# Performance work log

Hardware: AMD Instinct MI355X
Metric: run time of the kernel (lower is better)

Reference implementation:

```python
import jax, jax.numpy as jnp
import numpy as np

OBS, PRED, NAG, FIN, FOUT, H, NH, FF, NL = 8, 4, 256, 2, 2, 128, 8, 2048, 6


def _lin(x, w, b):
    return x @ w.T + b


def _ln(x, g, b, e=1e-5):
    m = x.mean(-1, keepdims=True)
    v = x.var(-1, keepdims=True)
    return (x - m) / jnp.sqrt(v + e) * g + b


def setup_inputs():
    key = jax.random.key(0)
    ks = iter(jax.random.split(key, 64))

    def w(shape, fan_in):
        return jax.random.normal(next(ks), shape, jnp.float32) / np.float32(np.sqrt(fan_in))

    return dict(
        traj_in=jax.random.normal(next(ks), (OBS + PRED, NAG, FIN), jnp.float32),
        adj_in=jax.random.uniform(next(ks), (OBS, NAG, NAG), jnp.float32),
        eps=jax.random.normal(next(ks), (OBS * NAG, H), jnp.float32),
        pro1_w=w((H, FIN), FIN), pro1_b=jnp.zeros(H, jnp.float32),
        pro2_w=w((H, H), H), pro2_b=jnp.zeros(H, jnp.float32),
        mu_w=w((H, H), H), mu_b=jnp.zeros(H, jnp.float32),
        ls_w=w((H, H), H), ls_b=jnp.zeros(H, jnp.float32),
        gdl_w=w((H, H), H), gdl_b=jnp.zeros(H, jnp.float32),
        pro3_w=w((H, OBS), OBS), pro3_b=jnp.zeros(H, jnp.float32),
        pro4_w=w((OBS, H), H), pro4_b=jnp.zeros(OBS, jnp.float32),
        pro5_w=w((FOUT, H), H), pro5_b=jnp.zeros(FOUT, jnp.float32),
        t_qkv_w=w((NL, 3 * H, H), H), t_qkv_b=jnp.zeros((NL, 3 * H), jnp.float32),
        t_out_w=w((NL, H, H), H), t_out_b=jnp.zeros((NL, H), jnp.float32),
        t_ff1_w=w((NL, FF, H), H), t_ff1_b=jnp.zeros((NL, FF), jnp.float32),
        t_ff2_w=w((NL, H, FF), FF), t_ff2_b=jnp.zeros((NL, H), jnp.float32),
        t_ln1_g=jnp.ones((NL, H), jnp.float32), t_ln1_b=jnp.zeros((NL, H), jnp.float32),
        t_ln2_g=jnp.ones((NL, H), jnp.float32), t_ln2_b=jnp.zeros((NL, H), jnp.float32),
        iftrain=1,
    )


def reference(traj_in, adj_in, eps, pro1_w, pro1_b, pro2_w, pro2_b, mu_w, mu_b,
              ls_w, ls_b, gdl_w, gdl_b, pro3_w, pro3_b, pro4_w, pro4_b,
              pro5_w, pro5_b, t_qkv_w, t_qkv_b, t_out_w, t_out_b,
              t_ff1_w, t_ff1_b, t_ff2_w, t_ff2_b, t_ln1_g, t_ln1_b,
              t_ln2_g, t_ln2_b, iftrain):
    batch_in = traj_in[:OBS, :, :FIN]            # [T, N, Fin]
    tar_y = traj_in[OBS:, :, :FOUT]              # [PRED, N, Fout]

    # block-diagonal adjacency over time, min-max normalized
    A = jax.scipy.linalg.block_diag(*[adj_in[t] for t in range(OBS)])  # [TN, TN]
    ADJ = (A - A.min()) / (A.max() - A.min())

    # GCNConv normalization: add remaining self-loops (weight 1), symmetric D^-1/2 A D^-1/2
    d = jnp.diagonal(ADJ)
    A_sl = ADJ + jnp.diag(jnp.where(d == 0, 1.0, 0.0).astype(ADJ.dtype))
    deg = A_sl.sum(0)
    dis = jnp.where(deg > 0, 1.0 / jnp.sqrt(deg), 0.0)
    agg = (dis[:, None] * A_sl * dis[None, :]).T  # aggregate src(row)->tgt(col)

    enc = _lin(jax.nn.relu(_lin(batch_in, pro1_w, pro1_b)), pro2_w, pro2_b)
    enc = enc.reshape(-1, H)                     # [TN, H]

    # VGAE encode (two GCNConv heads) + reparametrize, PyG clamps logstd at 10
    mu = agg @ _lin(enc, mu_w, mu_b)
    logstd = jnp.minimum(agg @ _lin(enc, ls_w, ls_b), 10.0)
    Z = jnp.where(jnp.asarray(iftrain) > 0, mu + eps * jnp.exp(logstd), mu)
    kld = -0.5 * jnp.mean(jnp.sum(1.0 + 2.0 * logstd - mu ** 2 - jnp.exp(2.0 * logstd), axis=1))

    out = _lin(Z, gdl_w, gdl_b)
    logits = Z @ Z.T                             # [TN, TN]
    struct_loss = jnp.mean(jnp.maximum(logits, 0.0) - logits * ADJ
                           + jnp.log1p(jnp.exp(-jnp.abs(logits))))

    # transformer over agents: [N, H, T] -> pro3 -> [N(seq), H(batch), H(d)]
    x = _lin(out.reshape(OBS, NAG, H).transpose(1, 2, 0), pro3_w, pro3_b)
    dh = H // NH
    S, B = x.shape[0], x.shape[1]
    for l in range(NL):
        qkv = _lin(x, t_qkv_w[l], t_qkv_b[l])
        q, k, v = jnp.split(qkv, 3, axis=-1)
        q = q.reshape(S, B, NH, dh)
        k = k.reshape(S, B, NH, dh)
        v = v.reshape(S, B, NH, dh)
        sc = jnp.einsum('sbhd,tbhd->bhst', q, k) / np.float32(np.sqrt(dh))
        att = jax.nn.softmax(sc, axis=-1)
        o = jnp.einsum('bhst,tbhd->sbhd', att, v).reshape(S, B, H)
        x = _ln(x + _lin(o, t_out_w[l], t_out_b[l]), t_ln1_g[l], t_ln1_b[l])
        f = _lin(jax.nn.relu(_lin(x, t_ff1_w[l], t_ff1_b[l])), t_ff2_w[l], t_ff2_b[l])
        x = _ln(x + f, t_ln2_g[l], t_ln2_b[l])

    out = _lin(x, pro4_w, pro4_b).transpose(2, 0, 1)   # [T, N, H]
    tra = _lin(out, pro5_w, pro5_b)                    # [T, N, Fout]
    traj = tra[-PRED:]
    traj_loss = jnp.sqrt(jnp.sum((traj - tar_y) ** 2, axis=-1)).sum(axis=0).mean()
    loss = traj_loss + kld + struct_loss
    return traj, loss
```

## Files before the change

### kernel.cpp

```cpp
#include <hip/hip_runtime.h>
#include <math.h>


namespace {

constexpr int kOBS = 8, kNAG = 256, kH = 128;
constexpr int kGN = kOBS * kNAG;
constexpr int kROWS = kNAG * kH;

typedef __attribute__((ext_vector_type(8))) short bf16x8;
typedef __attribute__((ext_vector_type(4))) float f32x4;
typedef __attribute__((ext_vector_type(4))) unsigned short us4;

struct Scal {
  int    mn_bits;
  int    mx_bits;
  float  Amin;
  float  invr;
  float  c0;
  int    pad;
  double kld_sum;
  double struct_sum;
  double traj_sum;
};

__device__ inline float waveReduceSum(float v) {
#pragma unroll
  for (int off = 32; off; off >>= 1) v += __shfl_xor(v, off, 64);
  return v;
}

__device__ inline unsigned short f2bf(float f) {
  unsigned u = __float_as_uint(f);
  return (unsigned short)((u + 0x7fffu + ((u >> 16) & 1u)) >> 16);
}
__device__ inline float bf2f(unsigned short h) {
  return __uint_as_float((unsigned)h << 16);
}
__device__ inline void split4(float4 v, us4& h, us4& l) {
  h.x = f2bf(v.x); l.x = f2bf(v.x - bf2f(h.x));
  h.y = f2bf(v.y); l.y = f2bf(v.y - bf2f(h.y));
  h.z = f2bf(v.z); l.z = f2bf(v.z - bf2f(h.z));
  h.w = f2bf(v.w); l.w = f2bf(v.w - bf2f(h.w));
}

__device__ inline int swz4(int c)  { return c ^ ((c >> 3) & 7); }
__device__ inline int swz16(int c) { return c ^ ((c >> 4) & 7); }

#define GLL(g, s)                                             \
  __builtin_amdgcn_global_load_lds(                           \
      (const __attribute__((address_space(1))) void*)(g),     \
      (__attribute__((address_space(3))) void*)(s), 16, 0, 0)

__global__ void k_init(Scal* sc) {
  if (threadIdx.x == 0) {
    sc->mn_bits = 0x7f800000;
    sc->mx_bits = 0xff800000;
    sc->kld_sum = 0.0;
    sc->struct_sum = 0.0;
    sc->traj_sum = 0.0;
  }
}

__global__ void k_minmax(const float* __restrict__ adj, int n, Scal* sc) {
  float lmin = INFINITY, lmax = -INFINITY;
  for (int i = blockIdx.x * blockDim.x + threadIdx.x; i < n;
       i += gridDim.x * blockDim.x) {
    float v = adj[i];
    lmin = fminf(lmin, v);
    lmax = fmaxf(lmax, v);
  }
#pragma unroll
  for (int off = 32; off; off >>= 1) {
    lmin = fminf(lmin, __shfl_xor(lmin, off, 64));
    lmax = fmaxf(lmax, __shfl_xor(lmax, off, 64));
  }
  __shared__ float smn[4], smx[4];
  int w = threadIdx.x >> 6;
  if ((threadIdx.x & 63) == 0) { smn[w] = lmin; smx[w] = lmax; }
  __syncthreads();
  if (threadIdx.x == 0) {
    lmin = fminf(fminf(smn[0], smn[1]), fminf(smn[2], smn[3]));
    lmax = fmaxf(fmaxf(smx[0], smx[1]), fmaxf(smx[2], smx[3]));
    atomicMin(&sc->mn_bits, __float_as_int(lmin));
    atomicMax(&sc->mx_bits, __float_as_int(lmax));
  }
}

__global__ void k_scale(Scal* sc) {
  float mn = fminf(0.0f, __int_as_float(sc->mn_bits));
  float mx = fmaxf(0.0f, __int_as_float(sc->mx_bits));
  sc->Amin = mn;
  sc->invr = 1.0f / (mx - mn);
  sc->c0 = (0.0f - mn) * sc->invr;
}

__global__ void k_dis(const float* __restrict__ adj, const Scal* __restrict__ sc,
                      float* __restrict__ dis) {
  int j = blockIdx.x * 256 + threadIdx.x;
  int t = j >> 8, jj = j & 255;
  const float* a = adj + (size_t)t * 65536;
  float Amin = sc->Amin, invr = sc->invr, c0 = sc->c0;
  float sum = 0.f;
  for (int i = 0; i < 256; ++i) sum += (a[i * 256 + jj] - Amin) * invr;
  float djj = (a[jj * 256 + jj] - Amin) * invr;
  float deg = sum + 1792.0f * c0 + (djj == 0.0f ? 1.0f : 0.0f);
  dis[j] = deg > 0.0f ? 1.0f / sqrtf(deg) : 0.0f;
}

__global__ void k_agg(const float* __restrict__ adj, const Scal* __restrict__ sc,
                      const float* __restrict__ dis, float* __restrict__ agg) {
  int idx = blockIdx.x * 256 + threadIdx.x;
  int t = idx >> 16, i = (idx >> 8) & 255, j = idx & 255;
  float v = (adj[(size_t)t * 65536 + j * 256 + i] - sc->Amin) * sc->invr;
  if (i == j && v == 0.0f) v += 1.0f;
  agg[idx] = dis[t * 256 + j] * v * dis[t * 256 + i];
}

__global__ void k_enc1(const float* __restrict__ traj, const float* __restrict__ w,
                       const float* __restrict__ b, float* __restrict__ out) {
  int idx = blockIdx.x * 256 + threadIdx.x;
  int r = idx >> 7, f = idx & 127;
  float v = traj[r * 2] * w[f * 2] + traj[r * 2 + 1] * w[f * 2 + 1] + b[f];
  out[idx] = fmaxf(v, 0.0f);
}

__global__ void k_cvt(const float* __restrict__ src, unsigned short* __restrict__ h,
                      unsigned short* __restrict__ l, int n4) {
  int i = blockIdx.x * 256 + threadIdx.x;
  if (i >= n4) return;
  float4 v = reinterpret_cast<const float4*>(src)[i];
  us4 hh, ll;
  split4(v, hh, ll);
  reinterpret_cast<us4*>(h)[i] = hh;
  reinterpret_cast<us4*>(l)[i] = ll;
}

#define BM 64
#define BN 64
#define KC 32
#define LP 68

template <bool TB>
__global__ __launch_bounds__(256) void gemm_kernel(
    const float* __restrict__ A, const float* __restrict__ B,
    const float* __restrict__ bias, float* __restrict__ C, int K, int ldb,
    int ldc, int flags, size_t aStride, size_t bStride, size_t cStride) {
  if (blockIdx.z) {
    A += (size_t)blockIdx.z * aStride;
    B += (size_t)blockIdx.z * bStride;
    C += (size_t)blockIdx.z * cStride;
  }
  __shared__ float As[KC][LP];
  __shared__ float Bs[KC][LP];
  const int tid = threadIdx.x;
  const int tx = tid & 15, ty = tid >> 4;
  const int m0 = blockIdx.y * BM, n0 = blockIdx.x * BN;
  float acc[4][4] = {};
  for (int k0 = 0; k0 < K; k0 += KC) {
#pragma unroll
    for (int i = 0; i < 2; ++i) {
      int q = tid + i * 256;
      int row = q >> 3, kq = q & 7;
      float4 v = *reinterpret_cast<const float4*>(
          &A[(size_t)(m0 + row) * K + k0 + kq * 4]);
      As[kq * 4 + 0][row] = v.x;
      As[kq * 4 + 1][row] = v.y;
      As[kq * 4 + 2][row] = v.z;
      As[kq * 4 + 3][row] = v.w;
    }
    if (TB) {
#pragma unroll
      for (int i = 0; i < 2; ++i) {
        int q = tid + i * 256;
        int row = q >> 3, kq = q & 7;
        float4 v = *reinterpret_cast<const float4*>(
            &B[(size_t)(n0 + row) * ldb + k0 + kq * 4]);
        Bs[kq * 4 + 0][row] = v.x;
        Bs[kq * 4 + 1][row] = v.y;
        Bs[kq * 4 + 2][row] = v.z;
        Bs[kq * 4 + 3][row] = v.w;
      }
    } else {
#pragma unroll
      for (int i = 0; i < 2; ++i) {
        int q = tid + i * 256;
        int kr = q >> 4, nq = q & 15;
        float4 v = *reinterpret_cast<const float4*>(
            &B[(size_t)(k0 + kr) * ldb + n0 + nq * 4]);
        *reinterpret_cast<float4*>(&Bs[kr][nq * 4]) = v;
      }
    }
    __syncthreads();
#pragma unroll
    for (int kk = 0; kk < KC; ++kk) {
      float4 a4 = *reinterpret_cast<const float4*>(&As[kk][ty * 4]);
      float4 b4 = *reinterpret_cast<const float4*>(&Bs[kk][tx * 4]);
      float av[4] = {a4.x, a4.y, a4.z, a4.w};
      float bv[4] = {b4.x, b4.y, b4.z, b4.w};
#pragma unroll
      for (int i = 0; i < 4; ++i)
#pragma unroll
        for (int j = 0; j < 4; ++j) acc[i][j] += av[i] * bv[j];
    }
    __syncthreads();
  }
  float bv[4] = {0.f, 0.f, 0.f, 0.f};
  if (bias) {
    float4 b4 = *reinterpret_cast<const float4*>(&bias[n0 + tx * 4]);
    bv[0] = b4.x; bv[1] = b4.y; bv[2] = b4.z; bv[3] = b4.w;
  }
#pragma unroll
  for (int i = 0; i < 4; ++i) {
    float* cp = &C[(size_t)(m0 + ty * 4 + i) * ldc + n0 + tx * 4];
    float4 o;
    float ov[4];
#pragma unroll
    for (int j = 0; j < 4; ++j) ov[j] = acc[i][j] + bv[j];
    if (flags & 2) {
      float4 old = *reinterpret_cast<const float4*>(cp);
      ov[0] += old.x; ov[1] += old.y; ov[2] += old.z; ov[3] += old.w;
    }
    if (flags & 1) {
#pragma unroll
      for (int j = 0; j < 4; ++j) ov[j] = fmaxf(ov[j], 0.0f);
    }
    o.x = ov[0]; o.y = ov[1]; o.z = ov[2]; o.w = ov[3];
    *reinterpret_cast<float4*>(cp) = o;
  }
}

template <int BMb, int BNb>
__global__ __launch_bounds__(256) void gemm_bf(
    const unsigned short* __restrict__ Ah, const unsigned short* __restrict__ Al,
    const unsigned short* __restrict__ Bh, const unsigned short* __restrict__ Bl,
    const float* __restrict__ bias, float* __restrict__ C,
    int K, int lda, int ldb, int ldc, int flags) {
  constexpr int MI = BMb / 32, NI = BNb / 32;
  constexpr int WTM = BMb / 2, WTN = BNb / 2;
  __shared__ unsigned short sAh[BMb * 32], sAl[BMb * 32];
  __shared__ unsigned short sBh[BNb * 32], sBl[BNb * 32];
  const int tid = threadIdx.x, lane = tid & 63, w = tid >> 6;
  const int wr = w >> 1, wc = w & 1;
  const int m0 = blockIdx.y * BMb, n0 = blockIdx.x * BNb;
  f32x4 acc[MI][NI];
#pragma unroll
  for (int i = 0; i < MI; ++i)
#pragma unroll
    for (int j = 0; j < NI; ++j) acc[i][j] = (f32x4){0.f, 0.f, 0.f, 0.f};

  for (int k0 = 0; k0 < K; k0 += 32) {
#pragma unroll
    for (int i = 0; i < BMb / 64; ++i) {
      int c = tid + i * 256;
      int g = swz4(c);
      int row = g >> 2, c4 = g & 3;
      size_t ga = (size_t)(m0 + row) * lda + k0 + c4 * 8;
      GLL(&Ah[ga], &sAh[c * 8]);
      GLL(&Al[ga], &sAl[c * 8]);
    }
#pragma unroll
    for (int i = 0; i < BNb / 64; ++i) {
      int c = tid + i * 256;
      int g = swz4(c);
      int row = g >> 2, c4 = g & 3;
      size_t ga = (size_t)(n0 + row) * ldb + k0 + c4 * 8;
      GLL(&Bh[ga], &sBh[c * 8]);
      GLL(&Bl[ga], &sBl[c * 8]);
    }
    __syncthreads();
    bf16x8 bh[NI], bl[NI];
#pragma unroll
    for (int ni = 0; ni < NI; ++ni) {
      int p = swz4((wc * WTN + ni * 16 + (lane & 15)) * 4 + (lane >> 4));
      bh[ni] = *reinterpret_cast<const bf16x8*>(&sBh[p * 8]);
      bl[ni] = *reinterpret_cast<const bf16x8*>(&sBl[p * 8]);
    }
#pragma unroll
    for (int mi = 0; mi < MI; ++mi) {
      int p = swz4((wr * WTM + mi * 16 + (lane & 15)) * 4 + (lane >> 4));
      bf16x8 ah = *reinterpret_cast<const bf16x8*>(&sAh[p * 8]);
      bf16x8 al = *reinterpret_cast<const bf16x8*>(&sAl[p * 8]);
#pragma unroll
      for (int ni = 0; ni < NI; ++ni) {
        acc[mi][ni] = __builtin_amdgcn_mfma_f32_16x16x32_bf16(
            ah, bh[ni], acc[mi][ni], 0, 0, 0);
        acc[mi][ni] = __builtin_amdgcn_mfma_f32_16x16x32_bf16(
            ah, bl[ni], acc[mi][ni], 0, 0, 0);
        acc[mi][ni] = __builtin_amdgcn_mfma_f32_16x16x32_bf16(
            al, bh[ni], acc[mi][ni], 0, 0, 0);
      }
    }
    __syncthreads();
  }
  const int crow0 = m0 + wr * WTM + (lane >> 4) * 4;
  const int ccol0 = n0 + wc * WTN + (lane & 15);
#pragma unroll
  for (int ni = 0; ni < NI; ++ni) {
    int col = ccol0 + ni * 16;
    float bv = bias ? bias[col] : 0.f;
#pragma unroll
    for (int mi = 0; mi < MI; ++mi) {
#pragma unroll
      for (int r = 0; r < 4; ++r) {
        int row = crow0 + mi * 16 + r;
        float v = acc[mi][ni][r] + bv;
        if (flags & 2) v += C[(size_t)row * ldc + col];
        if (flags & 1) v = fmaxf(v, 0.0f);
        C[(size_t)row * ldc + col] = v;
      }
    }
  }
}

__global__ __launch_bounds__(256) void k_ffn(
    const unsigned short* __restrict__ Xh, const unsigned short* __restrict__ Xl,
    const unsigned short* __restrict__ W1h, const unsigned short* __restrict__ W1l,
    const float* __restrict__ b1,
    const unsigned short* __restrict__ W2h, const unsigned short* __restrict__ W2l,
    const float* __restrict__ b2, float* __restrict__ out) {
  __shared__ unsigned short sXh[64 * 128], sXl[64 * 128];
  __shared__ unsigned short sW1h[32 * 128], sW1l[32 * 128];
  __shared__ unsigned short sPh[64 * 32], sPl[64 * 32];
  __shared__ unsigned short sW2h[128 * 32], sW2l[128 * 32];
  const int tid = threadIdx.x, lane = tid & 63, w = tid >> 6;
  const int wr = w >> 1, wc = w & 1;
  const int m0 = blockIdx.x * 64;
#pragma unroll
  for (int i = 0; i < 4; ++i) {
    int c = tid + i * 256;
    int g = swz16(c);
    size_t ga = (size_t)(m0 + (g >> 4)) * 128 + (g & 15) * 8;
    GLL(&Xh[ga], &sXh[c * 8]);
    GLL(&Xl[ga], &sXl[c * 8]);
  }
  __syncthreads();
  bf16x8 xah[4][2], xal[4][2];
#pragma unroll
  for (int ks = 0; ks < 4; ++ks)
#pragma unroll
    for (int mi = 0; mi < 2; ++mi) {
      int row = wr * 32 + mi * 16 + (lane & 15);
      int p = swz16(row * 16 + ks * 4 + (lane >> 4));
      xah[ks][mi] = *reinterpret_cast<const bf16x8*>(&sXh[p * 8]);
      xal[ks][mi] = *reinterpret_cast<const bf16x8*>(&sXl[p * 8]);
    }
  f32x4 acc2[2][4];
#pragma unroll
  for (int i = 0; i < 2; ++i)
#pragma unroll
    for (int j = 0; j < 4; ++j) acc2[i][j] = (f32x4){0.f, 0.f, 0.f, 0.f};

  const int pcol = wc * 16 + (lane & 15);
  for (int fc = 0; fc < 64; ++fc) {
    const int f0 = fc * 32;
#pragma unroll
    for (int i = 0; i < 2; ++i) {
      int c = tid + i * 256;
      {
        int g = swz16(c);
        size_t ga = (size_t)(f0 + (g >> 4)) * 128 + (g & 15) * 8;
        GLL(&W1h[ga], &sW1h[c * 8]);
        GLL(&W1l[ga], &sW1l[c * 8]);
      }
      {
        int g = swz4(c);
        size_t ga = (size_t)(g >> 2) * 2048 + f0 + (g & 3) * 8;
        GLL(&W2h[ga], &sW2h[c * 8]);
        GLL(&W2l[ga], &sW2l[c * 8]);
      }
    }
    __syncthreads();
    f32x4 acc1[2];
    acc1[0] = (f32x4){0.f, 0.f, 0.f, 0.f};
    acc1[1] = (f32x4){0.f, 0.f, 0.f, 0.f};
#pragma unroll
    for (int ks = 0; ks < 4; ++ks) {
      int p = swz16((wc * 16 + (lane & 15)) * 16 + ks * 4 + (lane >> 4));
      bf16x8 bh = *reinterpret_cast<const bf16x8*>(&sW1h[p * 8]);
      bf16x8 bl = *reinterpret_cast<const bf16x8*>(&sW1l[p * 8]);
#pragma unroll
      for (int mi = 0; mi < 2; ++mi) {
        acc1[mi] = __builtin_amdgcn_mfma_f32_16x16x32_bf16(xah[ks][mi], bh,
                                                           acc1[mi], 0, 0, 0);
        acc1[mi] = __builtin_amdgcn_mfma_f32_16x16x32_bf16(xah[ks][mi], bl,
                                                           acc1[mi], 0, 0, 0);
        acc1[mi] = __builtin_amdgcn_mfma_f32_16x16x32_bf16(xal[ks][mi], bh,
                                                           acc1[mi], 0, 0, 0);
      }
    }
    float b1v = b1[f0 + pcol];
#pragma unroll
    for (int mi = 0; mi < 2; ++mi)
#pragma unroll
      for (int r = 0; r < 4; ++r) {
        int prow = wr * 32 + mi * 16 + (lane >> 4) * 4 + r;
        float v = fmaxf(acc1[mi][r] + b1v, 0.0f);
        unsigned short h = f2bf(v);
        int p = swz4(prow * 4 + (pcol >> 3));
        sPh[p * 8 + (pcol & 7)] = h;
        sPl[p * 8 + (pcol & 7)] = f2bf(v - bf2f(h));
      }
    __syncthreads();
    bf16x8 pah[2], pal[2];
#pragma unroll
    for (int mi = 0; mi < 2; ++mi) {
      int p = swz4((wr * 32 + mi * 16 + (lane & 15)) * 4 + (lane >> 4));
      pah[mi] = *reinterpret_cast<const bf16x8*>(&sPh[p * 8]);
      pal[mi] = *reinterpret_cast<const bf16x8*>(&sPl[p * 8]);
    }
#pragma unroll
    for (int ni = 0; ni < 4; ++ni) {
      int p = swz4((wc * 64 + ni * 16 + (lane & 15)) * 4 + (lane >> 4));
      bf16x8 bh = *reinterpret_cast<const bf16x8*>(&sW2h[p * 8]);
      bf16x8 bl = *reinterpret_cast<const bf16x8*>(&sW2l[p * 8]);
#pragma unroll
      for (int mi = 0; mi < 2; ++mi) {
        acc2[mi][ni] = __builtin_amdgcn_mfma_f32_16x16x32_bf16(
            pah[mi], bh, acc2[mi][ni], 0, 0, 0);
        acc2[mi][ni] = __builtin_amdgcn_mfma_f32_16x16x32_bf16(
            pah[mi], bl, acc2[mi][ni], 0, 0, 0);
        acc2[mi][ni] = __builtin_amdgcn_mfma_f32_16x16x32_bf16(
            pal[mi], bh, acc2[mi][ni], 0, 0, 0);
      }
    }
    __syncthreads();
  }
#pragma unroll
  for (int ni = 0; ni < 4; ++ni) {
    int col = wc * 64 + ni * 16 + (lane & 15);
    float bv = b2[col];
#pragma unroll
    for (int mi = 0; mi < 2; ++mi)
#pragma unroll
      for (int r = 0; r < 4; ++r) {
        int row = m0 + wr * 32 + mi * 16 + (lane >> 4) * 4 + r;
        out[(size_t)row * 128 + col] = acc2[mi][ni][r] + bv;
      }
  }
}

__global__ void k_zkld(const float* __restrict__ mu, const float* __restrict__ lsr,
                       const float* __restrict__ eps, const int* __restrict__ iftrain,
                       float* __restrict__ Z, Scal* sc) {
  int i = blockIdx.x * 256 + threadIdx.x;
  float m = mu[i];
  float ls = fminf(lsr[i], 10.0f);
  float z = (*iftrain > 0) ? m + eps[i] * __expf(ls) : m;
  Z[i] = z;
  float kt = 1.0f + 2.0f * ls - m * m - __expf(2.0f * ls);
  kt = waveReduceSum(kt);
  __shared__ float sh[4];
  int w = threadIdx.x >> 6;
  if ((threadIdx.x & 63) == 0) sh[w] = kt;
  __syncthreads();
  if (threadIdx.x == 0)
    atomicAdd(&sc->kld_sum, (double)(sh[0] + sh[1] + sh[2] + sh[3]));
}

__global__ __launch_bounds__(256) void k_struct(const float* __restrict__ Z,
                                                const float* __restrict__ adj,
                                                Scal* sc) {
  __shared__ float As[KC][LP];
  __shared__ float Bs[KC][LP];
  const int tid = threadIdx.x;
  const int tx = tid & 15, ty = tid >> 4;
  const int m0 = blockIdx.y * BM, n0 = blockIdx.x * BN;
  float acc[4][4] = {};
  for (int k0 = 0; k0 < kH; k0 += KC) {
#pragma unroll
    for (int i = 0; i < 2; ++i) {
      int q = tid + i * 256;
      int row = q >> 3, kq = q & 7;
      float4 va = *reinterpret_cast<const float4*>(
          &Z[(size_t)(m0 + row) * kH + k0 + kq * 4]);
      As[kq * 4 + 0][row] = va.x;
      As[kq * 4 + 1][row] = va.y;
      As[kq * 4 + 2][row] = va.z;
      As[kq * 4 + 3][row] = va.w;
      float4 vb = *reinterpret_cast<const float4*>(
          &Z[(size_t)(n0 + row) * kH + k0 + kq * 4]);
      Bs[kq * 4 + 0][row] = vb.x;
      Bs[kq * 4 + 1][row] = vb.y;
      Bs[kq * 4 + 2][row] = vb.z;
      Bs[kq * 4 + 3][row] = vb.w;
    }
    __syncthreads();
#pragma unroll
    for (int kk = 0; kk < KC; ++kk) {
      float4 a4 = *reinterpret_cast<const float4*>(&As[kk][ty * 4]);
      float4 b4 = *reinterpret_cast<const float4*>(&Bs[kk][tx * 4]);
      float av[4] = {a4.x, a4.y, a4.z, a4.w};
      float bv[4] = {b4.x, b4.y, b4.z, b4.w};
#pragma unroll
      for (int i = 0; i < 4; ++i)
#pragma unroll
        for (int j = 0; j < 4; ++j) acc[i][j] += av[i] * bv[j];
    }
    __syncthreads();
  }
  float Amin = sc->Amin, invr = sc->invr, c0v = sc->c0;
  float lsum = 0.f;
#pragma unroll
  for (int i = 0; i < 4; ++i) {
#pragma unroll
    for (int j = 0; j < 4; ++j) {
      int gi = m0 + ty * 4 + i, gj = n0 + tx * 4 + j;
      float l = acc[i][j];
      float adjv = c0v;
      if ((gi >> 8) == (gj >> 8))
        adjv = (adj[((size_t)(gi >> 8) << 16) + (gi & 255) * 256 + (gj & 255)] -
                Amin) * invr;
      lsum += fmaxf(l, 0.0f) - l * adjv + __logf(1.0f + __expf(-fabsf(l)));
    }
  }
  lsum = waveReduceSum(lsum);
  __shared__ float sh[4];
  int w = threadIdx.x >> 6;
  if ((threadIdx.x & 63) == 0) sh[w] = lsum;
  __syncthreads();
  if (threadIdx.x == 0)
    atomicAdd(&sc->struct_sum, (double)(sh[0] + sh[1] + sh[2] + sh[3]));
}

__global__ void k_x0(const float* __restrict__ gdl, const float* __restrict__ w3,
                     const float* __restrict__ b3, float* __restrict__ X,
                     unsigned short* __restrict__ Xh,
                     unsigned short* __restrict__ Xl) {
  int f = threadIdx.x;
  size_t r = (size_t)blockIdx.x * 2 + threadIdx.y;
  int n = (int)(r >> 7), h = (int)(r & 127);
  float a = b3[f];
#pragma unroll
  for (int o = 0; o < 8; ++o)
    a += gdl[((size_t)o * 256 + n) * 128 + h] * w3[f * 8 + o];
  X[r * 128 + f] = a;
  unsigned short hh = f2bf(a);
  Xh[r * 128 + f] = hh;
  Xl[r * 128 + f] = f2bf(a - bf2f(hh));
}

__global__ __launch_bounds__(256) void k_attn(const float* __restrict__ QKV,
                                              unsigned short* __restrict__ Oh,
                                              unsigned short* __restrict__ Ol) {
  const int head = blockIdx.x, b = blockIdx.y;
  const int s = threadIdx.x;
  __shared__ float ks[256][16];
  __shared__ float vs[256][16];
  const size_t base = ((size_t)s * 128 + b) * 384 + head * 16;
#pragma unroll
  for (int i = 0; i < 4; ++i) {
    *reinterpret_cast<float4*>(&ks[s][i * 4]) =
        *reinterpret_cast<const float4*>(&QKV[base + 128 + i * 4]);
    *reinterpret_cast<float4*>(&vs[s][i * 4]) =
        *reinterpret_cast<const float4*>(&QKV[base + 256 + i * 4]);
  }
  float q[16];
#pragma unroll
  for (int i = 0; i < 4; ++i) {
    float4 v = *reinterpret_cast<const float4*>(&QKV[base + i * 4]);
    q[i * 4 + 0] = v.x * 0.25f; q[i * 4 + 1] = v.y * 0.25f;
    q[i * 4 + 2] = v.z * 0.25f; q[i * 4 + 3] = v.w * 0.25f;
  }
  __syncthreads();
  float m = -1e30f, lsum = 0.f;
  float o[16] = {};
#pragma unroll 2
  for (int t = 0; t < 256; ++t) {
    float kv[16], vv[16];
#pragma unroll
    for (int i = 0; i < 4; ++i) {
      float4 k4 = *reinterpret_cast<const float4*>(&ks[t][i * 4]);
      float4 v4 = *reinterpret_cast<const float4*>(&vs[t][i * 4]);
      kv[i * 4 + 0] = k4.x; kv[i * 4 + 1] = k4.y;
      kv[i * 4 + 2] = k4.z; kv[i * 4 + 3] = k4.w;
      vv[i * 4 + 0] = v4.x; vv[i * 4 + 1] = v4.y;
      vv[i * 4 + 2] = v4.z; vv[i * 4 + 3] = v4.w;
    }
    float d = 0.f;
#pragma unroll
    for (int i = 0; i < 16; ++i) d += q[i] * kv[i];
    if (d > m + 8.f) {
      float c = __expf(m - d);
      lsum *= c;
#pragma unroll
      for (int i = 0; i < 16; ++i) o[i] *= c;
      m = d;
    }
    float p = __expf(d - m);
    lsum += p;
#pragma unroll
    for (int i = 0; i < 16; ++i) o[i] += p * vv[i];
  }
  float inv = 1.0f / lsum;
  size_t ob = ((size_t)s * 128 + b) * 128 + head * 16;
#pragma unroll
  for (int i = 0; i < 4; ++i) {
    float4 v;
    v.x = o[i * 4 + 0] * inv; v.y = o[i * 4 + 1] * inv;
    v.z = o[i * 4 + 2] * inv; v.w = o[i * 4 + 3] * inv;
    us4 hh, ll;
    split4(v, hh, ll);
    *reinterpret_cast<us4*>(&Oh[ob + i * 4]) = hh;
    *reinterpret_cast<us4*>(&Ol[ob + i * 4]) = ll;
  }
}

__global__ __launch_bounds__(256) void k_resid_ln(
    float* __restrict__ X, const float* __restrict__ T,
    const float* __restrict__ g, const float* __restrict__ b,
    unsigned short* __restrict__ Xh, unsigned short* __restrict__ Xl) {
  int lane = threadIdx.x & 63, rl = threadIdx.x >> 6;
  size_t row = (size_t)blockIdx.x * 4 + rl;
  float* xp = X + row * 128;
  const float* tp = T + row * 128;
  float e0 = xp[lane] + tp[lane];
  float e1 = xp[lane + 64] + tp[lane + 64];
  float mean = waveReduceSum(e0 + e1) * 0.0078125f;
  float d0 = e0 - mean, d1 = e1 - mean;
  float var = waveReduceSum(d0 * d0 + d1 * d1) * 0.0078125f;
  float inv = 1.0f / sqrtf(var + 1e-5f);
  float v0 = d0 * inv * g[lane] + b[lane];
  float v1 = d1 * inv * g[lane + 64] + b[lane + 64];
  xp[lane] = v0;
  xp[lane + 64] = v1;
  unsigned short h0 = f2bf(v0), h1 = f2bf(v1);
  Xh[row * 128 + lane] = h0;
  Xl[row * 128 + lane] = f2bf(v0 - bf2f(h0));
  Xh[row * 128 + lane + 64] = h1;
  Xl[row * 128 + lane + 64] = f2bf(v1 - bf2f(h1));
}

__global__ void k_heady(const float* __restrict__ X, const float* __restrict__ w4,
                        const float* __restrict__ b4, float* __restrict__ y) {
  int tid = threadIdx.x;
  int o = tid & 7, rl = tid >> 3;
  size_t r = (size_t)blockIdx.x * 32 + rl;
  const float* xp = X + r * 128;
  const float* wp = w4 + o * 128;
  float a = b4[o];
  for (int f = 0; f < 128; f += 4)
    a += xp[f] * wp[f] + xp[f + 1] * wp[f + 1] + xp[f + 2] * wp[f + 2] +
         xp[f + 3] * wp[f + 3];
  y[r * 8 + o] = a;
}

__global__ void k_traj(const float* __restrict__ y, const float* __restrict__ w5,
                       const float* __restrict__ b5,
                       const float* __restrict__ traj_in, float* __restrict__ dout,
                       Scal* sc) {
  int n = blockIdx.x, lane = threadIdx.x;
  float w0a = w5[lane], w0b = w5[lane + 64];
  float w1a = w5[128 + lane], w1b = w5[128 + lane + 64];
  float dsum = 0.f;
  for (int oi = 0; oi < 4; ++oi) {
    int o = 4 + oi;
    float ya = y[((size_t)n * 128 + lane) * 8 + o];
    float yb = y[((size_t)n * 128 + lane + 64) * 8 + o];
    float s0 = waveReduceSum(w0a * ya + w0b * yb);
    float s1 = waveReduceSum(w1a * ya + w1b * yb);
    if (lane == 0) {
      float t0 = s0 + b5[0], t1 = s1 + b5[1];
      dout[oi * 512 + n * 2 + 0] = t0;
      dout[oi * 512 + n * 2 + 1] = t1;
      float dx = t0 - traj_in[((8 + oi) * 256 + n) * 2 + 0];
      float dy = t1 - traj_in[((8 + oi) * 256 + n) * 2 + 1];
      dsum += sqrtf(dx * dx + dy * dy);
    }
  }
  if (lane == 0) atomicAdd(&sc->traj_sum, (double)dsum);
}

__global__ void k_loss(const Scal* sc, float* dout) {
  if (threadIdx.x == 0) {
    double traj_loss = sc->traj_sum / 256.0;
    double kld = -0.5 * sc->kld_sum / 2048.0;
    double st = sc->struct_sum / (2048.0 * 2048.0);
    dout[2048] = (float)(traj_loss + kld + st);
  }
}

}

extern "C" void kernel_launch(void* const* d_in, const int* in_sizes, int n_in,
                              void* d_out, int out_size, void* d_ws,
                              size_t ws_size, hipStream_t stream) {
  (void)in_sizes; (void)n_in; (void)out_size; (void)ws_size;
  const float* traj_in = (const float*)d_in[0];
  const float* adj     = (const float*)d_in[1];
  const float* eps     = (const float*)d_in[2];
  const float* pro1_w  = (const float*)d_in[3];
  const float* pro1_b  = (const float*)d_in[4];
  const float* pro2_w  = (const float*)d_in[5];
  const float* pro2_b  = (const float*)d_in[6];
  const float* mu_w    = (const float*)d_in[7];
  const float* mu_b    = (const float*)d_in[8];
  const float* ls_w    = (const float*)d_in[9];
  const float* ls_b    = (const float*)d_in[10];
  const float* gdl_w   = (const float*)d_in[11];
  const float* gdl_b   = (const float*)d_in[12];
  const float* pro3_w  = (const float*)d_in[13];
  const float* pro3_b  = (const float*)d_in[14];
  const float* pro4_w  = (const float*)d_in[15];
  const float* pro4_b  = (const float*)d_in[16];
  const float* pro5_w  = (const float*)d_in[17];
  const float* pro5_b  = (const float*)d_in[18];
  const float* qkv_w   = (const float*)d_in[19];
  const float* qkv_b   = (const float*)d_in[20];
  const float* outp_w  = (const float*)d_in[21];
  const float* outp_b  = (const float*)d_in[22];
  const float* ff1_w   = (const float*)d_in[23];
  const float* ff1_b   = (const float*)d_in[24];
  const float* ff2_w   = (const float*)d_in[25];
  const float* ff2_b   = (const float*)d_in[26];
  const float* ln1_g   = (const float*)d_in[27];
  const float* ln1_b   = (const float*)d_in[28];
  const float* ln2_g   = (const float*)d_in[29];
  const float* ln2_b   = (const float*)d_in[30];
  const int*   iftrain = (const int*)d_in[31];
  float* dout = (float*)d_out;

  char* wsb = (char*)d_ws;
  size_t off = 0;
  auto alloc = [&](size_t bytes) {
    char* p = wsb + off;
    off += (bytes + 255) & ~(size_t)255;
    return p;
  };
  Scal* sc    = (Scal*)alloc(256);
  float* dis  = (float*)alloc(kGN * 4);
  float* agg  = (float*)alloc((size_t)kOBS * 65536 * 4);
  float* enc1 = (float*)alloc((size_t)kGN * kH * 4);
  float* enc  = (float*)alloc((size_t)kGN * kH * 4);
  float* Mmu  = (float*)alloc((size_t)kGN * kH * 4);
  float* Mls  = (float*)alloc((size_t)kGN * kH * 4);
  float* mu   = (float*)alloc((size_t)kGN * kH * 4);
  float* lsb  = (float*)alloc((size_t)kGN * kH * 4);
  float* Z    = (float*)alloc((size_t)kGN * kH * 4);
  float* gdl  = (float*)alloc((size_t)kGN * kH * 4);
  float* X    = (float*)alloc((size_t)kROWS * kH * 4);
  unsigned short* Xh = (unsigned short*)alloc((size_t)kROWS * kH * 2);
  unsigned short* Xl = (unsigned short*)alloc((size_t)kROWS * kH * 2);
  float* QKV = (float*)alloc((size_t)kROWS * 384 * 4);
  unsigned short* Oh = (unsigned short*)alloc((size_t)kROWS * kH * 2);
  unsigned short* Ol = (unsigned short*)alloc((size_t)kROWS * kH * 2);
  float* tmp  = (float*)alloc((size_t)kROWS * kH * 4);
  float* y    = (float*)alloc((size_t)kROWS * 8 * 4);
  unsigned short* qkvWh = (unsigned short*)alloc(6 * 384 * 128 * 2);
  unsigned short* qkvWl = (unsigned short*)alloc(6 * 384 * 128 * 2);
  unsigned short* outWh = (unsigned short*)alloc(6 * 128 * 128 * 2);
  unsigned short* outWl = (unsigned short*)alloc(6 * 128 * 128 * 2);
  unsigned short* ff1Wh = (unsigned short*)alloc(6 * 2048 * 128 * 2);
  unsigned short* ff1Wl = (unsigned short*)alloc(6 * 2048 * 128 * 2);
  unsigned short* ff2Wh = (unsigned short*)alloc(6 * 128 * 2048 * 2);
  unsigned short* ff2Wl = (unsigned short*)alloc(6 * 128 * 2048 * 2);

  auto gemm_nt_small = [&](const float* A, const float* B, const float* bias,
                           float* C, int M, int N, int K, int ldb, int ldc,
                           int flags) {
    dim3 g(N / 64, M / 64, 1);
    gemm_kernel<true><<<g, 256, 0, stream>>>(A, B, bias, C, K, ldb, ldc, flags,
                                             (size_t)0, (size_t)0, (size_t)0);
  };

  k_cvt<<<(6 * 384 * 128 / 4 + 255) / 256, 256, 0, stream>>>(
      qkv_w, qkvWh, qkvWl, 6 * 384 * 128 / 4);
  k_cvt<<<(6 * 128 * 128 / 4 + 255) / 256, 256, 0, stream>>>(
      outp_w, outWh, outWl, 6 * 128 * 128 / 4);
  k_cvt<<<(6 * 2048 * 128 / 4 + 255) / 256, 256, 0, stream>>>(
      ff1_w, ff1Wh, ff1Wl, 6 * 2048 * 128 / 4);
  k_cvt<<<(6 * 128 * 2048 / 4 + 255) / 256, 256, 0, stream>>>(
      ff2_w, ff2Wh, ff2Wl, 6 * 128 * 2048 / 4);

  k_init<<<1, 64, 0, stream>>>(sc);
  k_minmax<<<512, 256, 0, stream>>>(adj, kOBS * kNAG * kNAG, sc);
  k_scale<<<1, 1, 0, stream>>>(sc);
  k_dis<<<8, 256, 0, stream>>>(adj, sc, dis);
  k_agg<<<2048, 256, 0, stream>>>(adj, sc, dis, agg);

  k_enc1<<<(kGN * kH) / 256, 256, 0, stream>>>(traj_in, pro1_w, pro1_b, enc1);
  gemm_nt_small(enc1, pro2_w, pro2_b, enc, kGN, kH, kH, kH, kH, 0);
  gemm_nt_small(enc, mu_w, mu_b, Mmu, kGN, kH, kH, kH, kH, 0);
  gemm_nt_small(enc, ls_w, ls_b, Mls, kGN, kH, kH, kH, kH, 0);
  {
    dim3 g(kH / 64, kNAG / 64, kOBS);
    gemm_kernel<false><<<g, 256, 0, stream>>>(agg, Mmu, nullptr, mu, kNAG, kH,
                                              kH, 0, (size_t)65536,
                                              (size_t)kNAG * kH, (size_t)kNAG * kH);
    gemm_kernel<false><<<g, 256, 0, stream>>>(agg, Mls, nullptr, lsb, kNAG, kH,
                                              kH, 0, (size_t)65536,
                                              (size_t)kNAG * kH, (size_t)kNAG * kH);
  }
  k_zkld<<<(kGN * kH) / 256, 256, 0, stream>>>(mu, lsb, eps, iftrain, Z, sc);
  gemm_nt_small(Z, gdl_w, gdl_b, gdl, kGN, kH, kH, kH, kH, 0);
  k_struct<<<dim3(kGN / 64, kGN / 64), 256, 0, stream>>>(Z, adj, sc);
  k_x0<<<kROWS / 2, dim3(128, 2), 0, stream>>>(gdl, pro3_w, pro3_b, X, Xh, Xl);

  for (int l = 0; l < 6; ++l) {
    gemm_bf<128, 128><<<dim3(3, kROWS / 128), 256, 0, stream>>>(
        Xh, Xl, qkvWh + (size_t)l * 384 * 128, qkvWl + (size_t)l * 384 * 128,
        qkv_b + l * 384, QKV, 128, 128, 128, 384, 0);
    k_attn<<<dim3(8, 128), 256, 0, stream>>>(QKV, Oh, Ol);
    gemm_bf<64, 128><<<dim3(1, kROWS / 64), 256, 0, stream>>>(
        Oh, Ol, outWh + (size_t)l * 128 * 128, outWl + (size_t)l * 128 * 128,
        outp_b + l * 128, tmp, 128, 128, 128, 128, 0);
    k_resid_ln<<<kROWS / 4, 256, 0, stream>>>(X, tmp, ln1_g + l * kH,
                                              ln1_b + l * kH, Xh, Xl);
    k_ffn<<<kROWS / 64, 256, 0, stream>>>(
        Xh, Xl, ff1Wh + (size_t)l * 2048 * 128, ff1Wl + (size_t)l * 2048 * 128,
        ff1_b + l * 2048, ff2Wh + (size_t)l * 128 * 2048,
        ff2Wl + (size_t)l * 128 * 2048, ff2_b + l * 128, tmp);
    k_resid_ln<<<kROWS / 4, 256, 0, stream>>>(X, tmp, ln2_g + l * kH,
                                              ln2_b + l * kH, Xh, Xl);
  }

  k_heady<<<kROWS / 32, 256, 0, stream>>>(X, pro4_w, pro4_b, y);
  k_traj<<<kNAG, 64, 0, stream>>>(y, pro5_w, pro5_b, traj_in, dout, sc);
  k_loss<<<1, 1, 0, stream>>>(sc, dout);
}
```

Baseline: 1.974 ms.

## Double-buffer FFN weight tiles in LDS with explicit waitcnt pipelining

Restructures the fused FFN kernel to double-buffer the W1/W2 chunk loads into one shared LDS arena, so the next 32-wide feature chunk is prefetched while the current one is computed. It replaces __syncthreads with explicit vmcnt/lgkmcnt waits plus s_barrier, and stages the b1 bias into LDS once instead of reading it from global memory on every chunk. The aim is to hide global-to-LDS latency behind the MFMA work. In exchange it relies on hand-counted vmcnt values, which risks races if the count of outstanding loads is wrong, and it raises LDS use per block.

```diff
diff --git a/kernel.cpp b/kernel.cpp
--- a/kernel.cpp
+++ b/kernel.cpp
@@ -319,66 +319,106 @@
     const float* __restrict__ b1,
     const unsigned short* __restrict__ W2h, const unsigned short* __restrict__ W2l,
     const float* __restrict__ b2, float* __restrict__ out) {
-  __shared__ unsigned short sXh[64 * 128], sXl[64 * 128];
-  __shared__ unsigned short sW1h[32 * 128], sW1l[32 * 128];
-  __shared__ unsigned short sPh[64 * 32], sPl[64 * 32];
-  __shared__ unsigned short sW2h[128 * 32], sW2l[128 * 32];
+  __shared__ unsigned short sLds[40960];
+  unsigned short* sPh = sLds + 32768;
+  unsigned short* sPl = sLds + 34816;
+  float* sB1 = reinterpret_cast<float*>(sLds + 36864);
   const int tid = threadIdx.x, lane = tid & 63, w = tid >> 6;
   const int wr = w >> 1, wc = w & 1;
   const int m0 = blockIdx.x * 64;
-#pragma unroll
-  for (int i = 0; i < 4; ++i) {
-    int c = tid + i * 256;
-    int g = swz16(c);
-    size_t ga = (size_t)(m0 + (g >> 4)) * 128 + (g & 15) * 8;
-    GLL(&Xh[ga], &sXh[c * 8]);
-    GLL(&Xl[ga], &sXl[c * 8]);
-  }
-  __syncthreads();
-  bf16x8 xah[4][2], xal[4][2];
-#pragma unroll
-  for (int ks = 0; ks < 4; ++ks)
-#pragma unroll
-    for (int mi = 0; mi < 2; ++mi) {
-      int row = wr * 32 + mi * 16 + (lane & 15);
-      int p = swz16(row * 16 + ks * 4 + (lane >> 4));
-      xah[ks][mi] = *reinterpret_cast<const bf16x8*>(&sXh[p * 8]);
-      xal[ks][mi] = *reinterpret_cast<const bf16x8*>(&sXl[p * 8]);
-    }
-  f32x4 acc2[2][4];
-#pragma unroll
-  for (int i = 0; i < 2; ++i)
-#pragma unroll
-    for (int j = 0; j < 4; ++j) acc2[i][j] = (f32x4){0.f, 0.f, 0.f, 0.f};
-
-  const int pcol = wc * 16 + (lane & 15);
-  for (int fc = 0; fc < 64; ++fc) {
-    const int f0 = fc * 32;
+
+  auto stageW = [&](int buf, int f0) {
+    unsigned short* d = sLds + buf * 16384;
 #pragma unroll
     for (int i = 0; i < 2; ++i) {
       int c = tid + i * 256;
       {
         int g = swz16(c);
         size_t ga = (size_t)(f0 + (g >> 4)) * 128 + (g & 15) * 8;
-        GLL(&W1h[ga], &sW1h[c * 8]);
-        GLL(&W1l[ga], &sW1l[c * 8]);
+        GLL(&W1h[ga], &d[c * 8]);
+        GLL(&W1l[ga], &d[4096 + c * 8]);
       }
       {
         int g = swz4(c);
         size_t ga = (size_t)(g >> 2) * 2048 + f0 + (g & 3) * 8;
-        GLL(&W2h[ga], &sW2h[c * 8]);
-        GLL(&W2l[ga], &sW2l[c * 8]);
-      }
-    }
-    __syncthreads();
+        GLL(&W2h[ga], &d[8192 + c * 8]);
+        GLL(&W2l[ga], &d[12288 + c * 8]);
+      }
+    }
+  };
+
+  {
+    unsigned short* sXh = sLds + 16384;
+    unsigned short* sXl = sLds + 24576;
+#pragma unroll
+    for (int i = 0; i < 4; ++i) {
+      int c = tid + i * 256;
+      int g = swz16(c);
+      size_t ga = (size_t)(m0 + (g >> 4)) * 128 + (g & 15) * 8;
+      GLL(&Xh[ga], &sXh[c * 8]);
+      GLL(&Xl[ga], &sXl[c * 8]);
+    }
+#pragma unroll
+    for (int i = 0; i < 2; ++i) {
+      int c = tid + i * 256;
+      GLL(&b1[c * 4], &sB1[c * 4]);
+    }
+  }
+  __builtin_amdgcn_sched_barrier(0);
+  asm volatile("s_waitcnt vmcnt(0)");
+  __builtin_amdgcn_sched_barrier(0);
+  __builtin_amdgcn_s_barrier();
+  stageW(0, 0);
+  bf16x8 xah[4][2], xal[4][2];
+  {
+    unsigned short* sXh = sLds + 16384;
+    unsigned short* sXl = sLds + 24576;
+#pragma unroll
+    for (int ks = 0; ks < 4; ++ks)
+#pragma unroll
+      for (int mi = 0; mi < 2; ++mi) {
+        int row = wr * 32 + mi * 16 + (lane & 15);
+        int p = swz16(row * 16 + ks * 4 + (lane >> 4));
+        xah[ks][mi] = *reinterpret_cast<const bf16x8*>(&sXh[p * 8]);
+        xal[ks][mi] = *reinterpret_cast<const bf16x8*>(&sXl[p * 8]);
+      }
+  }
+  __builtin_amdgcn_sched_barrier(0);
+  asm volatile("s_waitcnt lgkmcnt(0)");
+  __builtin_amdgcn_sched_barrier(0);
+  __builtin_amdgcn_s_barrier();
+
+  f32x4 acc2[2][4];
+#pragma unroll
+  for (int i = 0; i < 2; ++i)
+#pragma unroll
+    for (int j = 0; j < 4; ++j) acc2[i][j] = (f32x4){0.f, 0.f, 0.f, 0.f};
+
+  const int pcol = wc * 16 + (lane & 15);
+
+  auto body = [&](int cur, int f0, bool hasNext) {
+    unsigned short* bW1h = sLds + cur * 16384;
+    unsigned short* bW1l = bW1h + 4096;
+    unsigned short* bW2h = bW1h + 8192;
+    unsigned short* bW2l = bW1h + 12288;
+    if (hasNext) {
+      stageW(cur ^ 1, f0 + 32);
+      __builtin_amdgcn_sched_barrier(0);
+      asm volatile("s_waitcnt vmcnt(8)");
+    } else {
+      __builtin_amdgcn_sched_barrier(0);
+      asm volatile("s_waitcnt vmcnt(0)");
+    }
+    __builtin_amdgcn_sched_barrier(0);
+    __builtin_amdgcn_s_barrier();
     f32x4 acc1[2];
     acc1[0] = (f32x4){0.f, 0.f, 0.f, 0.f};
     acc1[1] = (f32x4){0.f, 0.f, 0.f, 0.f};
 #pragma unroll
     for (int ks = 0; ks < 4; ++ks) {
       int p = swz16((wc * 16 + (lane & 15)) * 16 + ks * 4 + (lane >> 4));
-      bf16x8 bh = *reinterpret_cast<const bf16x8*>(&sW1h[p * 8]);
-      bf16x8 bl = *reinterpret_cast<const bf16x8*>(&sW1l[p * 8]);
+      bf16x8 bh = *reinterpret_cast<const bf16x8*>(&bW1h[p * 8]);
+      bf16x8 bl = *reinterpret_cast<const bf16x8*>(&bW1l[p * 8]);
 #pragma unroll
       for (int mi = 0; mi < 2; ++mi) {
         acc1[mi] = __builtin_amdgcn_mfma_f32_16x16x32_bf16(xah[ks][mi], bh,
@@ -389,7 +429,7 @@
                                                            acc1[mi], 0, 0, 0);
       }
     }
-    float b1v = b1[f0 + pcol];
+    float b1v = sB1[f0 + pcol];
 #pragma unroll
     for (int mi = 0; mi < 2; ++mi)
 #pragma unroll
@@ -401,7 +441,10 @@
         sPh[p * 8 + (pcol & 7)] = h;
         sPl[p * 8 + (pcol & 7)] = f2bf(v - bf2f(h));
       }
-    __syncthreads();
+    __builtin_amdgcn_sched_barrier(0);
+    asm volatile("s_waitcnt lgkmcnt(0)");
+    __builtin_amdgcn_sched_barrier(0);
+    __builtin_amdgcn_s_barrier();
     bf16x8 pah[2], pal[2];
 #pragma unroll
     for (int mi = 0; mi < 2; ++mi) {
@@ -412,8 +455,8 @@
 #pragma unroll
     for (int ni = 0; ni < 4; ++ni) {
       int p = swz4((wc * 64 + ni * 16 + (lane & 15)) * 4 + (lane >> 4));
-      bf16x8 bh = *reinterpret_cast<const bf16x8*>(&sW2h[p * 8]);
-      bf16x8 bl = *reinterpret_cast<const bf16x8*>(&sW2l[p * 8]);
+      bf16x8 bh = *reinterpret_cast<const bf16x8*>(&bW2h[p * 8]);
+      bf16x8 bl = *reinterpret_cast<const bf16x8*>(&bW2l[p * 8]);
 #pragma unroll
       for (int mi = 0; mi < 2; ++mi) {
         acc2[mi][ni] = __builtin_amdgcn_mfma_f32_16x16x32_bf16(
@@ -424,8 +467,15 @@
             pal[mi], bh, acc2[mi][ni], 0, 0, 0);
       }
     }
-    __syncthreads();
-  }
+    __builtin_amdgcn_sched_barrier(0);
+    __builtin_amdgcn_s_barrier();
+  };
+
+  for (int fc2 = 0; fc2 < 32; ++fc2) {
+    body(0, fc2 * 64, true);
+    body(1, fc2 * 64 + 32, fc2 != 31);
+  }
+
 #pragma unroll
   for (int ni = 0; ni < 4; ++ni) {
     int col = wc * 64 + ni * 16 + (lane & 15);
```

Measured after the change: 1.913 ms. -3.1%, faster.
